# Performance work log

Hardware: AMD Instinct MI355X
Metric: run time of the kernel (lower is better)

## Reference

```python
import jax, jax.numpy as jnp
import numpy as np

N, E, F_IN, DIM, G = 50000, 800000, 128, 128, 512
NUM_GC_LAYERS = 3
S2S_STEPS = 3


def setup_inputs() -> dict:
    key = jax.random.key(0)
    ks = jax.random.split(key, 17)
    s = 0.05
    rn = lambda k, shape: jax.random.normal(k, shape, jnp.float32) * s
    x = jax.random.normal(ks[0], (N, F_IN), jnp.float32)
    edge_index = jax.random.randint(ks[1], (2, E), 0, N)
    batch = jnp.sort(jax.random.randint(ks[2], (N,), 0, G))
    return dict(
        x=x, edge_index=edge_index, batch=batch,
        lin0_W=rn(ks[3], (DIM, F_IN)), lin0_b=rn(ks[4], (DIM,)),
        gin_W1=rn(ks[5], (DIM, DIM)), gin_b1=rn(ks[6], (DIM,)),
        gin_W2=rn(ks[7], (DIM, DIM)), gin_b2=rn(ks[8], (DIM,)),
        gru_Wih=rn(ks[9], (3 * DIM, DIM)), gru_Whh=rn(ks[10], (3 * DIM, DIM)),
        gru_bih=rn(ks[11], (3 * DIM,)), gru_bhh=rn(ks[12], (3 * DIM,)),
        lstm_Wih=rn(ks[13], (4 * DIM, 2 * DIM)), lstm_Whh=rn(ks[14], (4 * DIM, DIM)),
        lstm_bih=rn(ks[15], (4 * DIM,)), lstm_bhh=rn(ks[16], (4 * DIM,)),
    )


def reference(x, edge_index, batch, lin0_W, lin0_b, gin_W1, gin_b1, gin_W2, gin_b2,
              gru_Wih, gru_Whh, gru_bih, gru_bhh,
              lstm_Wih, lstm_Whh, lstm_bih, lstm_bhh):
    src, dst = edge_index[0], edge_index[1]
    out = jax.nn.relu(x @ lin0_W.T + lin0_b)          # [N, DIM]
    h = out                                            # GRU hidden (seq_len=1, 1 layer)
    for _ in range(NUM_GC_LAYERS):
        # GINConv, eps=0: nn(x + sum_{j in N(i)} x_j); scatter-add over edge list
        aggr = jax.ops.segment_sum(out[src], dst, num_segments=N)
        z = out + aggr
        m = jax.nn.relu(jax.nn.relu(z @ gin_W1.T + gin_b1) @ gin_W2.T + gin_b2)
        # single GRU step (PyTorch gate order: r, z, n)
        gx = m @ gru_Wih.T + gru_bih
        gh = h @ gru_Whh.T + gru_bhh
        gxr, gxz, gxn = jnp.split(gx, 3, axis=-1)
        ghr, ghz, ghn = jnp.split(gh, 3, axis=-1)
        r = jax.nn.sigmoid(gxr + ghr)
        zt = jax.nn.sigmoid(gxz + ghz)
        n = jnp.tanh(gxn + r * ghn)
        h = (1.0 - zt) * n + zt * h
        out = h
    # Set2Set pooling (processing_steps=3), LSTM(2*DIM -> DIM), gate order i,f,g,o
    q_star = jnp.zeros((G, 2 * DIM), x.dtype)
    hl = jnp.zeros((G, DIM), x.dtype)
    cl = jnp.zeros((G, DIM), x.dtype)
    for _ in range(S2S_STEPS):
        gates = q_star @ lstm_Wih.T + lstm_bih + hl @ lstm_Whh.T + lstm_bhh
        i, f, g, o = jnp.split(gates, 4, axis=-1)
        cl = jax.nn.sigmoid(f) * cl + jax.nn.sigmoid(i) * jnp.tanh(g)
        hl = jax.nn.sigmoid(o) * jnp.tanh(cl)
        q = hl                                          # [G, DIM]
        e = jnp.sum(out * q[batch], axis=-1)            # [N] attention logits
        emax = jax.lax.stop_gradient(jax.ops.segment_max(e, batch, num_segments=G))
        emax = jnp.where(jnp.isfinite(emax), emax, 0.0)
        a_num = jnp.exp(e - emax[batch])
        denom = jax.ops.segment_sum(a_num, batch, num_segments=G)
        a = a_num / (denom[batch] + 1e-16)              # per-graph softmax
        rvec = jax.ops.segment_sum(a[:, None] * out, batch, num_segments=G)
        q_star = jnp.concatenate([q, rvec], axis=-1)    # [G, 2*DIM]
    return (q_star, out)
```

## Files before the change

kernel.cpp:

```cpp
#include <hip/hip_runtime.h>
#include <hip/hip_bf16.h>
#include <math.h>

static constexpr int NN  = 50000;
static constexpr int NE  = 800000;
static constexpr int DIM = 128;
static constexpr int NG  = 512;
static constexpr int NBLK = (NN + 255) / 256;

typedef __attribute__((ext_vector_type(8))) short bf16x8;
typedef __attribute__((ext_vector_type(4))) float f32x4;
typedef __attribute__((ext_vector_type(8))) float f32x8;

__device__ __forceinline__ float sigm(float x) {
    return __builtin_amdgcn_rcpf(1.0f + __expf(-x));
}
__device__ __forceinline__ float ftanh(float x) {
    x = fminf(fmaxf(x, -15.f), 15.f);
    float t = __expf(2.f * x);
    return (t - 1.f) * __builtin_amdgcn_rcpf(t + 1.f);
}
__device__ __forceinline__ float b2f(ushort u) { return __uint_as_float(((unsigned)u) << 16); }
__device__ __forceinline__ ushort f2b(float f) {
    __hip_bfloat16 h = __float2bfloat16(f);
    return *reinterpret_cast<ushort*>(&h);
}
__device__ __forceinline__ bf16x8 ldb8(const ushort* p) {
    return *reinterpret_cast<const bf16x8*>(p);
}
__device__ __forceinline__ f32x8 acc8(f32x8 a, uint4 v) {
    a[0] += b2f(v.x & 0xffff); a[1] += b2f(v.x >> 16);
    a[2] += b2f(v.y & 0xffff); a[3] += b2f(v.y >> 16);
    a[4] += b2f(v.z & 0xffff); a[5] += b2f(v.z >> 16);
    a[6] += b2f(v.w & 0xffff); a[7] += b2f(v.w >> 16);
    return a;
}

__global__ __launch_bounds__(256) void k_prep(const float* __restrict__ lin0_W,
                                              const float* __restrict__ gin_W1,
                                              const float* __restrict__ gin_W2,
                                              const float* __restrict__ gru_Wih,
                                              const float* __restrict__ gru_Whh,
                                              const float* __restrict__ gru_bih,
                                              const float* __restrict__ gru_bhh,
                                              const float* __restrict__ lstm_Wih,
                                              const float* __restrict__ lstm_Whh,
                                              const float* __restrict__ lstm_bih,
                                              const float* __restrict__ lstm_bhh,
                                              const int* __restrict__ batch,
                                              ushort* __restrict__ wlin0,
                                              ushort* __restrict__ wg1,
                                              ushort* __restrict__ wg2,
                                              ushort* __restrict__ wihb,
                                              ushort* __restrict__ whhb,
                                              ushort* __restrict__ wrz,
                                              float* __restrict__ brz,
                                              float* __restrict__ wltr,
                                              float* __restrict__ bl,
                                              int* __restrict__ deg,
                                              int* __restrict__ gstart,
                                              float* __restrict__ zf) {
    const int S0 = 16384, S1 = S0 + 16384, S2 = S1 + 16384;
    const int S3 = S2 + 49152, S4 = S3 + 49152, S5 = S4 + 65536;
    const int S6 = S5 + 256, S7 = S6 + 196608, S8 = S7 + 512;
    const int S9 = S8 + (NN + 1), S10 = S9 + (NG + 1), S11 = S10 + 262144;
    int i = blockIdx.x * 256 + threadIdx.x;
    if (i < S0) { wlin0[i] = f2b(lin0_W[i]); }
    else if (i < S1) { int j = i - S0; wg1[j] = f2b(gin_W1[j]); }
    else if (i < S2) { int j = i - S1; wg2[j] = f2b(gin_W2[j]); }
    else if (i < S3) { int j = i - S2; wihb[j] = f2b(gru_Wih[j]); }
    else if (i < S4) { int j = i - S3; whhb[j] = f2b(gru_Whh[j]); }
    else if (i < S5) {
        int j = i - S4; int col = j >> 8, k = j & 255;
        int row = (col >> 7) * 128 + (col & 127);
        wrz[j] = f2b((k < 128) ? gru_Whh[row * 128 + k] : gru_Wih[row * 128 + (k - 128)]);
    }
    else if (i < S6) { int j = i - S5; brz[j] = gru_bih[j] + gru_bhh[j]; }
    else if (i < S7) {
        int j = i - S6; int k = j / 512, col = j % 512;
        wltr[j] = (k < 256) ? lstm_Wih[(size_t)col * 256 + k]
                            : lstm_Whh[(size_t)col * 128 + (k - 256)];
    }
    else if (i < S8) { int j = i - S7; bl[j] = lstm_bih[j] + lstm_bhh[j]; }
    else if (i < S9) { deg[i - S8] = 0; }
    else if (i < S10) {
        int g = i - S9;
        int lo = 0, hi = NN;
        while (lo < hi) { int mid = (lo + hi) >> 1; if (batch[mid] < g) lo = mid + 1; else hi = mid; }
        gstart[g] = lo;
    }
    else if (i < S11) { zf[i - S10] = 0.f; }
}
static constexpr int PREP_TOTAL = 16384 * 3 + 49152 * 2 + 65536 + 256 + 196608 + 512 + (NN + 1) + (NG + 1) + 262144;

__global__ void k_count(const int* __restrict__ dst, int* __restrict__ deg, int e) {
    int i = blockIdx.x * blockDim.x + threadIdx.x;
    if (i < e) atomicAdd(&deg[dst[i]], 1);
}

__global__ __launch_bounds__(256) void k_scan_blk(const int* __restrict__ deg,
                                                  int* __restrict__ part,
                                                  int* __restrict__ blksum) {
    __shared__ int s[256];
    int b = blockIdx.x, t = threadIdx.x;
    int i = b * 256 + t;
    int v = (i < NN) ? deg[i] : 0;
    s[t] = v;
    __syncthreads();
    #pragma unroll
    for (int off = 1; off < 256; off <<= 1) {
        int x = (t >= off) ? s[t - off] : 0;
        __syncthreads();
        s[t] += x;
        __syncthreads();
    }
    if (i < NN) part[i] = s[t] - v;
    if (t == 255) blksum[b] = s[255];
}
__global__ __launch_bounds__(256) void k_scan_top(const int* __restrict__ blksum,
                                                  int* __restrict__ blkoff) {
    __shared__ int s[256];
    int t = threadIdx.x;
    int v = (t < NBLK) ? blksum[t] : 0;
    s[t] = v;
    __syncthreads();
    #pragma unroll
    for (int off = 1; off < 256; off <<= 1) {
        int x = (t >= off) ? s[t - off] : 0;
        __syncthreads();
        s[t] += x;
        __syncthreads();
    }
    if (t < NBLK) blkoff[t] = s[t] - v;
    if (t == NBLK - 1) blkoff[NBLK] = s[t];
}
__global__ __launch_bounds__(256) void k_scan_add(const int* __restrict__ part,
                                                  const int* __restrict__ blkoff,
                                                  int* __restrict__ rowptr,
                                                  int* __restrict__ bcur) {
    int b = blockIdx.x, t = threadIdx.x;
    int i = b * 256 + t;
    if (i < NN) {
        int r = part[i] + blkoff[b];
        rowptr[i] = r;
        if ((i & 255) == 0) bcur[i >> 8] = r;
    }
    if (b == 0 && t == 0) rowptr[NN] = blkoff[NBLK];
}

__global__ __launch_bounds__(256) void k_bucket(const int* __restrict__ src,
                                                const int* __restrict__ dst,
                                                int* __restrict__ bcur,
                                                int2* __restrict__ pairs, int e) {
    __shared__ int lcnt[256];
    __shared__ int lbase[256];
    int tid = threadIdx.x;
    lcnt[tid] = 0;
    __syncthreads();
    int base = blockIdx.x * 4096;
    #pragma unroll
    for (int k = 0; k < 16; ++k) {
        int e0 = base + k * 256 + tid;
        if (e0 < e) atomicAdd(&lcnt[dst[e0] >> 8], 1);
    }
    __syncthreads();
    int cnt = lcnt[tid];
    if (cnt > 0) lbase[tid] = atomicAdd(&bcur[tid], cnt);
    __syncthreads();
    lcnt[tid] = 0;
    __syncthreads();
    #pragma unroll
    for (int k = 0; k < 16; ++k) {
        int e0 = base + k * 256 + tid;
        if (e0 < e) {
            int d = dst[e0];
            int b = d >> 8;
            int off = atomicAdd(&lcnt[b], 1);
            pairs[lbase[b] + off] = make_int2(src[e0], d);
        }
    }
}
__global__ __launch_bounds__(256) void k_fillbkt(const int2* __restrict__ pairs,
                                                 const int* __restrict__ rowptr,
                                                 int* __restrict__ csr) {
    __shared__ int lcur[256];
    int b = blockIdx.x, tid = threadIdx.x;
    int w0 = b << 8;
    int w1 = min(w0 + 256, NN);
    if (w0 + tid < w1) lcur[tid] = rowptr[w0 + tid];
    __syncthreads();
    int r0 = rowptr[w0], r1 = rowptr[w1];
    for (int i = r0 + tid; i < r1; i += 256) {
        int2 p = pairs[i];
        int pos = atomicAdd(&lcur[p.y - w0], 1);
        csr[pos] = p.x;
    }
}

__global__ __launch_bounds__(256) void k_lin0(const float* __restrict__ X,
                                              const ushort* __restrict__ W,
                                              const float* __restrict__ bias,
                                              ushort* __restrict__ AB, int n) {
    int lane = threadIdx.x & 63, wave = threadIdx.x >> 6;
    int c0 = lane & 15, kg = (lane >> 4) * 8;
    int tb0 = wave * 32;
    bf16x8 B[2][4];
    #pragma unroll
    for (int t = 0; t < 2; ++t)
        #pragma unroll
        for (int kk = 0; kk < 4; ++kk)
            B[t][kk] = ldb8(W + (size_t)(tb0 + t * 16 + c0) * 128 + kk * 32 + kg);

    for (int m0 = blockIdx.x * 64; m0 < n; m0 += gridDim.x * 64) {
        f32x4 acc[4][2];
        #pragma unroll
        for (int m = 0; m < 4; ++m) { acc[m][0] = {0,0,0,0}; acc[m][1] = {0,0,0,0}; }
        #pragma unroll
        for (int kk = 0; kk < 4; ++kk) {
            #pragma unroll
            for (int m = 0; m < 4; ++m) {
                int ar = min(m0 + m * 16 + c0, n - 1);
                const float* a = X + (size_t)ar * 128 + kk * 32 + kg;
                float4 x0 = *reinterpret_cast<const float4*>(a);
                float4 x1 = *reinterpret_cast<const float4*>(a + 4);
                bf16x8 af;
                af[0] = (short)f2b(x0.x); af[1] = (short)f2b(x0.y);
                af[2] = (short)f2b(x0.z); af[3] = (short)f2b(x0.w);
                af[4] = (short)f2b(x1.x); af[5] = (short)f2b(x1.y);
                af[6] = (short)f2b(x1.z); af[7] = (short)f2b(x1.w);
                acc[m][0] = __builtin_amdgcn_mfma_f32_16x16x32_bf16(af, B[0][kk], acc[m][0], 0, 0, 0);
                acc[m][1] = __builtin_amdgcn_mfma_f32_16x16x32_bf16(af, B[1][kk], acc[m][1], 0, 0, 0);
            }
        }
        #pragma unroll
        for (int m = 0; m < 4; ++m) {
            int rbase = m0 + m * 16 + ((lane >> 4) << 2);
            #pragma unroll
            for (int t = 0; t < 2; ++t) {
                int col = tb0 + t * 16 + c0;
                float bv = bias[col];
                #pragma unroll
                for (int j = 0; j < 4; ++j) {
                    int row = rbase + j;
                    if (row < n) {
                        float v = fmaxf(acc[m][t][j] + bv, 0.f);
                        AB[(size_t)row * 128 + col] = f2b(v);
                    }
                }
            }
        }
    }
}

__global__ __launch_bounds__(512) void k_aggmlp(const ushort* __restrict__ AB,
                                                const int* __restrict__ rowptr,
                                                const int* __restrict__ csr,
                                                const ushort* __restrict__ W1,
                                                const float* __restrict__ b1,
                                                const ushort* __restrict__ W2,
                                                const float* __restrict__ b2,
                                                ushort* __restrict__ mt, int n) {
    __shared__ ushort Z_lds[32 * 136];
    __shared__ ushort M_lds[32 * 136];
    int tid = threadIdx.x;
    int lane = tid & 63, wave = tid >> 6;
    int c0 = lane & 15, kg = (lane >> 4) * 8;
    int colw = wave * 16 + c0;
    int rj = (lane >> 4) << 2;
    int grow_r = tid >> 4;
    int segi = tid & 15;
    const int stride = gridDim.x * 32;

    bf16x8 B1[4], B2[4];
    #pragma unroll
    for (int kk = 0; kk < 4; ++kk) {
        B1[kk] = ldb8(W1 + (size_t)colw * 128 + kk * 32 + kg);
        B2[kk] = ldb8(W2 + (size_t)colw * 128 + kk * 32 + kg);
    }
    float bv1 = b1[colw], bv2 = b2[colw];
    const uint4* bp = (const uint4*)AB;

    for (int m0 = blockIdx.x * 32; m0 < n; m0 += stride) {
        f32x8 A0 = {0,0,0,0,0,0,0,0};
        int grow = m0 + grow_r;
        if (grow < n) {
            f32x8 A1 = {0,0,0,0,0,0,0,0}, A2 = {0,0,0,0,0,0,0,0}, A3 = {0,0,0,0,0,0,0,0};
            A0 = acc8(A0, bp[(size_t)grow * 16 + segi]);
            int p = rowptr[grow], p1 = rowptr[grow + 1];
            for (; p + 4 <= p1; p += 4) {
                uint4 v0 = bp[(size_t)csr[p + 0] * 16 + segi];
                uint4 v1 = bp[(size_t)csr[p + 1] * 16 + segi];
                uint4 v2 = bp[(size_t)csr[p + 2] * 16 + segi];
                uint4 v3 = bp[(size_t)csr[p + 3] * 16 + segi];
                A0 = acc8(A0, v0); A1 = acc8(A1, v1);
                A2 = acc8(A2, v2); A3 = acc8(A3, v3);
            }
            for (; p < p1; ++p) A0 = acc8(A0, bp[(size_t)csr[p] * 16 + segi]);
            #pragma unroll
            for (int i = 0; i < 8; ++i) A0[i] += A1[i] + A2[i] + A3[i];
        }
        bf16x8 zz;
        #pragma unroll
        for (int i = 0; i < 8; ++i) zz[i] = (short)f2b(A0[i]);
        *reinterpret_cast<bf16x8*>(&Z_lds[grow_r * 136 + segi * 8]) = zz;
        __syncthreads();
        {
            f32x4 a[2] = {{0,0,0,0},{0,0,0,0}};
            #pragma unroll
            for (int kk = 0; kk < 4; ++kk) {
                bf16x8 f0 = *reinterpret_cast<const bf16x8*>(&Z_lds[c0 * 136 + kk * 32 + kg]);
                bf16x8 f1 = *reinterpret_cast<const bf16x8*>(&Z_lds[(16 + c0) * 136 + kk * 32 + kg]);
                a[0] = __builtin_amdgcn_mfma_f32_16x16x32_bf16(f0, B1[kk], a[0], 0, 0, 0);
                a[1] = __builtin_amdgcn_mfma_f32_16x16x32_bf16(f1, B1[kk], a[1], 0, 0, 0);
            }
            #pragma unroll
            for (int m = 0; m < 2; ++m)
                #pragma unroll
                for (int j = 0; j < 4; ++j)
                    M_lds[(m * 16 + rj + j) * 136 + colw] = f2b(fmaxf(a[m][j] + bv1, 0.f));
        }
        __syncthreads();
        {
            f32x4 a[2] = {{0,0,0,0},{0,0,0,0}};
            #pragma unroll
            for (int kk = 0; kk < 4; ++kk) {
                bf16x8 f0 = *reinterpret_cast<const bf16x8*>(&M_lds[c0 * 136 + kk * 32 + kg]);
                bf16x8 f1 = *reinterpret_cast<const bf16x8*>(&M_lds[(16 + c0) * 136 + kk * 32 + kg]);
                a[0] = __builtin_amdgcn_mfma_f32_16x16x32_bf16(f0, B2[kk], a[0], 0, 0, 0);
                a[1] = __builtin_amdgcn_mfma_f32_16x16x32_bf16(f1, B2[kk], a[1], 0, 0, 0);
            }
            #pragma unroll
            for (int m = 0; m < 2; ++m)
                #pragma unroll
                for (int j = 0; j < 4; ++j) {
                    int gr2 = m0 + m * 16 + rj + j;
                    if (gr2 < n)
                        mt[(size_t)gr2 * 128 + colw] = f2b(fmaxf(a[m][j] + bv2, 0.f));
                }
        }
        __syncthreads();
    }
}

template<bool WRITEH>
__global__ __launch_bounds__(512) void k_gru3b(const ushort* __restrict__ ABin,
                                               const ushort* __restrict__ mt,
                                               const ushort* __restrict__ wrz,
                                               const float* __restrict__ brz,
                                               const ushort* __restrict__ Wn,
                                               const ushort* __restrict__ Un,
                                               const float* __restrict__ bin,
                                               const float* __restrict__ bhn,
                                               float* __restrict__ Hf,
                                               ushort* __restrict__ ABout, int n) {
    __shared__ ushort A_lds[32 * 264];
    int tid = threadIdx.x;
    int lane = tid & 63, wave = tid >> 6;
    int c0 = lane & 15, kg = (lane >> 4) * 8;
    int colw = wave * 16 + c0;
    int rj = (lane >> 4) << 2;
    int srow = tid >> 4, scol = (tid & 15) * 8;
    const int stride = gridDim.x * 32;

    bf16x8 Brz[2][8];
    #pragma unroll
    for (int kk = 0; kk < 8; ++kk) {
        Brz[0][kk] = ldb8(wrz + (size_t)(colw) * 256 + kk * 32 + kg);
        Brz[1][kk] = ldb8(wrz + (size_t)(128 + colw) * 256 + kk * 32 + kg);
    }
    bf16x8 Bn[4], Bu[4];
    #pragma unroll
    for (int kk = 0; kk < 4; ++kk) {
        Bn[kk] = ldb8(Wn + (size_t)colw * 128 + kk * 32 + kg);
        Bu[kk] = ldb8(Un + (size_t)colw * 128 + kk * 32 + kg);
    }
    float biN = bin[colw], bhN = bhn[colw];
    float brzR = brz[colw], brzZ = brz[128 + colw];

    int m0 = blockIdx.x * 32;
    bf16x8 ph, pm;
    if (m0 < n) {
        int gr = min(m0 + srow, n - 1);
        ph = ldb8(ABin + (size_t)gr * 128 + scol);
        pm = ldb8(mt + (size_t)gr * 128 + scol);
    }
    for (; m0 < n; m0 += stride) {
        *reinterpret_cast<bf16x8*>(&A_lds[srow * 264 + scol]) = ph;
        *reinterpret_cast<bf16x8*>(&A_lds[srow * 264 + 128 + scol]) = pm;
        __syncthreads();
        int mn = m0 + stride;
        if (mn < n) {
            int gr = min(mn + srow, n - 1);
            ph = ldb8(ABin + (size_t)gr * 128 + scol);
            pm = ldb8(mt + (size_t)gr * 128 + scol);
        }
        f32x4 aR[2] = {{0,0,0,0},{0,0,0,0}};
        f32x4 aZ[2] = {{0,0,0,0},{0,0,0,0}};
        #pragma unroll
        for (int kk = 0; kk < 8; ++kk) {
            bf16x8 f0 = *reinterpret_cast<const bf16x8*>(&A_lds[c0 * 264 + kk * 32 + kg]);
            bf16x8 f1 = *reinterpret_cast<const bf16x8*>(&A_lds[(16 + c0) * 264 + kk * 32 + kg]);
            aR[0] = __builtin_amdgcn_mfma_f32_16x16x32_bf16(f0, Brz[0][kk], aR[0], 0, 0, 0);
            aZ[0] = __builtin_amdgcn_mfma_f32_16x16x32_bf16(f0, Brz[1][kk], aZ[0], 0, 0, 0);
            aR[1] = __builtin_amdgcn_mfma_f32_16x16x32_bf16(f1, Brz[0][kk], aR[1], 0, 0, 0);
            aZ[1] = __builtin_amdgcn_mfma_f32_16x16x32_bf16(f1, Brz[1][kk], aZ[1], 0, 0, 0);
        }
        f32x4 an[2] = {{0,0,0,0},{0,0,0,0}};
        f32x4 au[2] = {{0,0,0,0},{0,0,0,0}};
        #pragma unroll
        for (int kk = 0; kk < 4; ++kk) {
            bf16x8 am0 = *reinterpret_cast<const bf16x8*>(&A_lds[c0 * 264 + 128 + kk * 32 + kg]);
            bf16x8 ah0 = *reinterpret_cast<const bf16x8*>(&A_lds[c0 * 264 + kk * 32 + kg]);
            bf16x8 am1 = *reinterpret_cast<const bf16x8*>(&A_lds[(16 + c0) * 264 + 128 + kk * 32 + kg]);
            bf16x8 ah1 = *reinterpret_cast<const bf16x8*>(&A_lds[(16 + c0) * 264 + kk * 32 + kg]);
            an[0] = __builtin_amdgcn_mfma_f32_16x16x32_bf16(am0, Bn[kk], an[0], 0, 0, 0);
            au[0] = __builtin_amdgcn_mfma_f32_16x16x32_bf16(ah0, Bu[kk], au[0], 0, 0, 0);
            an[1] = __builtin_amdgcn_mfma_f32_16x16x32_bf16(am1, Bn[kk], an[1], 0, 0, 0);
            au[1] = __builtin_amdgcn_mfma_f32_16x16x32_bf16(ah1, Bu[kk], au[1], 0, 0, 0);
        }
        #pragma unroll
        for (int m = 0; m < 2; ++m)
            #pragma unroll
            for (int j = 0; j < 4; ++j) {
                int row = m * 16 + rj + j;
                int grow = m0 + row;
                if (grow < n) {
                    float r  = sigm(aR[m][j] + brzR);
                    float zt = sigm(aZ[m][j] + brzZ);
                    float hold = b2f(A_lds[row * 264 + colw]);
                    float nn = ftanh(an[m][j] + biN + r * (au[m][j] + bhN));
                    float hn = (1.f - zt) * nn + zt * hold;
                    ABout[(size_t)grow * 128 + colw] = f2b(hn);
                    if (WRITEH) Hf[(size_t)grow * 128 + colw] = hn;
                }
            }
        __syncthreads();
    }
}

__global__ __launch_bounds__(512) void k_s2s(const ushort* __restrict__ AB,
                                             const float* __restrict__ Wt,
                                             const float* __restrict__ bl,
                                             const int* __restrict__ gstart,
                                             const float* __restrict__ qstar,
                                             float* __restrict__ hl,
                                             float* __restrict__ cl,
                                             float* __restrict__ qout) {
    int g = blockIdx.x, tid = threadIdx.x, lane = tid & 63, wave = tid >> 6;
    __shared__ float qh[384];
    __shared__ float gbuf[512];
    __shared__ float q[128];
    __shared__ float wm[8];
    __shared__ float sw[8];
    __shared__ float rv[8][128];
    if (tid < 256) qh[tid] = qstar[(size_t)g * 256 + tid];
    else if (tid < 384) qh[tid] = hl[(size_t)g * 128 + (tid - 256)];
    __syncthreads();
    float acc = bl[tid];
    #pragma unroll 8
    for (int k = 0; k < 384; ++k)
        acc += Wt[(size_t)k * 512 + tid] * qh[k];
    gbuf[tid] = acc;
    __syncthreads();
    if (tid < 128) {
        float iv = sigm(gbuf[tid]);
        float fv = sigm(gbuf[128 + tid]);
        float gv = ftanh(gbuf[256 + tid]);
        float ov = sigm(gbuf[384 + tid]);
        float cn = fv * cl[(size_t)g * 128 + tid] + iv * gv;
        cl[(size_t)g * 128 + tid] = cn;
        float hn = ov * ftanh(cn);
        hl[(size_t)g * 128 + tid] = hn;
        q[tid] = hn;
    }
    __syncthreads();
    int s = gstart[g], e = gstart[g + 1];
    float q0 = q[2 * lane], q1 = q[2 * lane + 1];
    float mx = -1e30f, sumw = 0.f, a0 = 0.f, a1 = 0.f;
    for (int node = s + wave; node < e; node += 8) {
        unsigned u = ((const unsigned*)AB)[(size_t)node * 64 + lane];
        float v0 = b2f(u & 0xffff), v1 = b2f(u >> 16);
        float p = v0 * q0 + v1 * q1;
        #pragma unroll
        for (int off = 1; off < 64; off <<= 1) p += __shfl_xor(p, off);
        float nm = fmaxf(mx, p);
        float corr = __expf(mx - nm);
        float wgt = __expf(p - nm);
        sumw = sumw * corr + wgt;
        a0 = a0 * corr + wgt * v0;
        a1 = a1 * corr + wgt * v1;
        mx = nm;
    }
    if (lane == 0) wm[wave] = mx;
    __syncthreads();
    float gm = fmaxf(fmaxf(fmaxf(wm[0], wm[1]), fmaxf(wm[2], wm[3])),
                     fmaxf(fmaxf(wm[4], wm[5]), fmaxf(wm[6], wm[7])));
    float cw = __expf(mx - gm);
    rv[wave][2 * lane] = a0 * cw;
    rv[wave][2 * lane + 1] = a1 * cw;
    if (lane == 0) sw[wave] = sumw * cw;
    __syncthreads();
    if (tid < 128) {
        float r = 0.f, d = 1e-16f;
        #pragma unroll
        for (int wv = 0; wv < 8; ++wv) r += rv[wv][tid];
        #pragma unroll
        for (int wv = 0; wv < 8; ++wv) d += sw[wv];
        qout[(size_t)g * 256 + tid] = q[tid];
        qout[(size_t)g * 256 + 128 + tid] = r / d;
    }
}

extern "C" void kernel_launch(void* const* d_in, const int* in_sizes, int n_in,
                              void* d_out, int out_size, void* d_ws, size_t ws_size,
                              hipStream_t stream) {
    const float* x        = (const float*)d_in[0];
    const int*   ei       = (const int*)d_in[1];
    const int*   batch    = (const int*)d_in[2];
    const float* lin0_W   = (const float*)d_in[3];
    const float* lin0_b   = (const float*)d_in[4];
    const float* gin_W1   = (const float*)d_in[5];
    const float* gin_b1   = (const float*)d_in[6];
    const float* gin_W2   = (const float*)d_in[7];
    const float* gin_b2   = (const float*)d_in[8];
    const float* gru_Wih  = (const float*)d_in[9];
    const float* gru_Whh  = (const float*)d_in[10];
    const float* gru_bih  = (const float*)d_in[11];
    const float* gru_bhh  = (const float*)d_in[12];
    const float* lstm_Wih = (const float*)d_in[13];
    const float* lstm_Whh = (const float*)d_in[14];
    const float* lstm_bih = (const float*)d_in[15];
    const float* lstm_bhh = (const float*)d_in[16];

    float* qstar_out = (float*)d_out;
    float* h         = (float*)d_out + (size_t)NG * 2 * DIM;

    char* w = (char*)d_ws;
    ushort* AB0   = (ushort*)w; w += (size_t)NN * 128 * 2;
    ushort* AB1   = (ushort*)w; w += (size_t)NN * 128 * 2;
    ushort* mt    = (ushort*)w; w += (size_t)NN * 128 * 2;
    ushort* wlin0 = (ushort*)w; w += 16384 * 2;
    ushort* wg1   = (ushort*)w; w += 16384 * 2;
    ushort* wg2   = (ushort*)w; w += 16384 * 2;
    ushort* wihb  = (ushort*)w; w += 49152 * 2;
    ushort* whhb  = (ushort*)w; w += 49152 * 2;
    ushort* wrz   = (ushort*)w; w += 65536 * 2;
    float* brz    = (float*)w;  w += 256 * 4;
    float* wltr   = (float*)w;  w += (size_t)512 * 384 * 4;
    float* bl     = (float*)w;  w += 512 * 4;
    float* qstar  = (float*)w;  w += (size_t)NG * 2 * DIM * 4;
    float* hl     = (float*)w;  w += (size_t)NG * DIM * 4;
    float* cl     = (float*)w;  w += (size_t)NG * DIM * 4;
    int* deg      = (int*)w;    w += (size_t)(NN + 1) * 4;
    int* rowptr   = (int*)w;    w += (size_t)(NN + 1) * 4;
    int* bcur     = (int*)w;    w += 256 * 4;
    int* csr_src  = (int*)w;    w += (size_t)NE * 4;
    int2* pairs   = (int2*)w;   w += (size_t)NE * 8;
    int* gstart   = (int*)w;    w += (size_t)(NG + 1) * 4;
    int* part     = (int*)w;    w += (size_t)NN * 4;
    int* blksum   = (int*)w;    w += (size_t)(NBLK + 1) * 4;
    int* blkoff   = (int*)w;    w += (size_t)(NBLK + 1) * 4;

    const int* src = ei;
    const int* dst = ei + NE;

    k_prep<<<(PREP_TOTAL + 255) / 256, 256, 0, stream>>>(
        lin0_W, gin_W1, gin_W2, gru_Wih, gru_Whh, gru_bih, gru_bhh,
        lstm_Wih, lstm_Whh, lstm_bih, lstm_bhh, batch,
        wlin0, wg1, wg2, wihb, whhb, wrz, brz, wltr, bl, deg, gstart, qstar);

    k_count<<<(NE + 255) / 256, 256, 0, stream>>>(dst, deg, NE);
    k_scan_blk<<<NBLK, 256, 0, stream>>>(deg, part, blksum);
    k_scan_top<<<1, 256, 0, stream>>>(blksum, blkoff);
    k_scan_add<<<NBLK, 256, 0, stream>>>(part, blkoff, rowptr, bcur);
    k_bucket<<<(NE + 4095) / 4096, 256, 0, stream>>>(src, dst, bcur, pairs, NE);
    k_fillbkt<<<NBLK, 256, 0, stream>>>(pairs, rowptr, csr_src);

    k_lin0<<<782, 256, 0, stream>>>(x, wlin0, lin0_b, AB0, NN);

    for (int t = 0; t < 3; ++t) {
        ushort* ABc = (t & 1) ? AB1 : AB0;
        ushort* ABn = (t & 1) ? AB0 : AB1;
        k_aggmlp<<<1024, 512, 0, stream>>>(ABc, rowptr, csr_src,
                                           wg1, gin_b1, wg2, gin_b2, mt, NN);
        if (t < 2)
            k_gru3b<false><<<512, 512, 0, stream>>>(ABc, mt, wrz, brz,
                                                    wihb + 256 * 128, whhb + 256 * 128,
                                                    gru_bih + 256, gru_bhh + 256, h, ABn, NN);
        else
            k_gru3b<true><<<512, 512, 0, stream>>>(ABc, mt, wrz, brz,
                                                   wihb + 256 * 128, whhb + 256 * 128,
                                                   gru_bih + 256, gru_bhh + 256, h, ABn, NN);
    }
    const ushort* ABfin = AB1;

    for (int st = 0; st < 3; ++st)
        k_s2s<<<NG, 512, 0, stream>>>(ABfin, wltr, bl, gstart, qstar, hl, cl,
                                      (st == 2) ? qstar_out : qstar);
}
```

Measured before the change: 398.7 us.

## Build CSR via bucket-level counts and fuse lin0 with bucketing

Replaces per-node degree counting and the three-kernel global scan with per-bucket counts, a single-block scan, and a local degree scan inside the fill kernel that writes rowptr. The bucketing pass and the lin0 GEMM now share one launch using disjoint block ranges. This removes several kernel launches and the global atomics on per-node degrees. The cost is that the fill kernel reads the pairs array twice, and lin0 blocks share the grid with bucketing blocks.

```diff
diff --git a/kernel.cpp b/kernel.cpp
--- a/kernel.cpp
+++ b/kernel.cpp
@@ -57,13 +57,13 @@
                                               float* __restrict__ brz,
                                               float* __restrict__ wltr,
                                               float* __restrict__ bl,
-                                              int* __restrict__ deg,
                                               int* __restrict__ gstart,
-                                              float* __restrict__ zf) {
+                                              float* __restrict__ zf,
+                                              int* __restrict__ bcnt) {
     const int S0 = 16384, S1 = S0 + 16384, S2 = S1 + 16384;
     const int S3 = S2 + 49152, S4 = S3 + 49152, S5 = S4 + 65536;
     const int S6 = S5 + 256, S7 = S6 + 196608, S8 = S7 + 512;
-    const int S9 = S8 + (NN + 1), S10 = S9 + (NG + 1), S11 = S10 + 262144;
+    const int S9 = S8 + (NG + 1), S10 = S9 + 262144, S11 = S10 + 256;
     int i = blockIdx.x * 256 + threadIdx.x;
     if (i < S0) { wlin0[i] = f2b(lin0_W[i]); }
     else if (i < S1) { int j = i - S0; wg1[j] = f2b(gin_W1[j]); }
@@ -82,125 +82,94 @@
                             : lstm_Whh[(size_t)col * 128 + (k - 256)];
     }
     else if (i < S8) { int j = i - S7; bl[j] = lstm_bih[j] + lstm_bhh[j]; }
-    else if (i < S9) { deg[i - S8] = 0; }
-    else if (i < S10) {
-        int g = i - S9;
+    else if (i < S9) {
+        int g = i - S8;
         int lo = 0, hi = NN;
         while (lo < hi) { int mid = (lo + hi) >> 1; if (batch[mid] < g) lo = mid + 1; else hi = mid; }
         gstart[g] = lo;
     }
-    else if (i < S11) { zf[i - S10] = 0.f; }
-}
-static constexpr int PREP_TOTAL = 16384 * 3 + 49152 * 2 + 65536 + 256 + 196608 + 512 + (NN + 1) + (NG + 1) + 262144;
-
-__global__ void k_count(const int* __restrict__ dst, int* __restrict__ deg, int e) {
-    int i = blockIdx.x * blockDim.x + threadIdx.x;
-    if (i < e) atomicAdd(&deg[dst[i]], 1);
-}
-
-__global__ __launch_bounds__(256) void k_scan_blk(const int* __restrict__ deg,
-                                                  int* __restrict__ part,
-                                                  int* __restrict__ blksum) {
-    __shared__ int s[256];
-    int b = blockIdx.x, t = threadIdx.x;
-    int i = b * 256 + t;
-    int v = (i < NN) ? deg[i] : 0;
-    s[t] = v;
-    __syncthreads();
-    #pragma unroll
-    for (int off = 1; off < 256; off <<= 1) {
-        int x = (t >= off) ? s[t - off] : 0;
-        __syncthreads();
-        s[t] += x;
-        __syncthreads();
-    }
-    if (i < NN) part[i] = s[t] - v;
-    if (t == 255) blksum[b] = s[255];
-}
-__global__ __launch_bounds__(256) void k_scan_top(const int* __restrict__ blksum,
-                                                  int* __restrict__ blkoff) {
-    __shared__ int s[256];
-    int t = threadIdx.x;
-    int v = (t < NBLK) ? blksum[t] : 0;
-    s[t] = v;
-    __syncthreads();
-    #pragma unroll
-    for (int off = 1; off < 256; off <<= 1) {
-        int x = (t >= off) ? s[t - off] : 0;
-        __syncthreads();
-        s[t] += x;
-        __syncthreads();
-    }
-    if (t < NBLK) blkoff[t] = s[t] - v;
-    if (t == NBLK - 1) blkoff[NBLK] = s[t];
-}
-__global__ __launch_bounds__(256) void k_scan_add(const int* __restrict__ part,
-                                                  const int* __restrict__ blkoff,
-                                                  int* __restrict__ rowptr,
-                                                  int* __restrict__ bcur) {
-    int b = blockIdx.x, t = threadIdx.x;
-    int i = b * 256 + t;
-    if (i < NN) {
-        int r = part[i] + blkoff[b];
-        rowptr[i] = r;
-        if ((i & 255) == 0) bcur[i >> 8] = r;
-    }
-    if (b == 0 && t == 0) rowptr[NN] = blkoff[NBLK];
-}
-
-__global__ __launch_bounds__(256) void k_bucket(const int* __restrict__ src,
-                                                const int* __restrict__ dst,
-                                                int* __restrict__ bcur,
-                                                int2* __restrict__ pairs, int e) {
-    __shared__ int lcnt[256];
-    __shared__ int lbase[256];
+    else if (i < S10) { zf[i - S9] = 0.f; }
+    else if (i < S11) { bcnt[i - S10] = 0; }
+}
+static constexpr int PREP_TOTAL = 16384 * 3 + 49152 * 2 + 65536 + 256 + 196608 + 512 + (NG + 1) + 262144 + 256;
+
+__global__ __launch_bounds__(256) void k_bcount(const int* __restrict__ dst,
+                                                int* __restrict__ bcnt, int e) {
+    __shared__ int l[256];
     int tid = threadIdx.x;
-    lcnt[tid] = 0;
+    l[tid] = 0;
     __syncthreads();
     int base = blockIdx.x * 4096;
     #pragma unroll
     for (int k = 0; k < 16; ++k) {
         int e0 = base + k * 256 + tid;
-        if (e0 < e) atomicAdd(&lcnt[dst[e0] >> 8], 1);
-    }
-    __syncthreads();
-    int cnt = lcnt[tid];
-    if (cnt > 0) lbase[tid] = atomicAdd(&bcur[tid], cnt);
-    __syncthreads();
-    lcnt[tid] = 0;
+        if (e0 < e) atomicAdd(&l[dst[e0] >> 8], 1);
+    }
+    __syncthreads();
+    if (l[tid] > 0) atomicAdd(&bcnt[tid], l[tid]);
+}
+
+__global__ __launch_bounds__(256) void k_btop(const int* __restrict__ bcnt,
+                                              int* __restrict__ bbase,
+                                              int* __restrict__ bcur) {
+    __shared__ int s[256];
+    int t = threadIdx.x;
+    int v = bcnt[t];
+    s[t] = v;
     __syncthreads();
     #pragma unroll
-    for (int k = 0; k < 16; ++k) {
-        int e0 = base + k * 256 + tid;
-        if (e0 < e) {
-            int d = dst[e0];
-            int b = d >> 8;
-            int off = atomicAdd(&lcnt[b], 1);
-            pairs[lbase[b] + off] = make_int2(src[e0], d);
-        }
-    }
-}
-__global__ __launch_bounds__(256) void k_fillbkt(const int2* __restrict__ pairs,
-                                                 const int* __restrict__ rowptr,
-                                                 int* __restrict__ csr) {
-    __shared__ int lcur[256];
-    int b = blockIdx.x, tid = threadIdx.x;
-    int w0 = b << 8;
-    int w1 = min(w0 + 256, NN);
-    if (w0 + tid < w1) lcur[tid] = rowptr[w0 + tid];
-    __syncthreads();
-    int r0 = rowptr[w0], r1 = rowptr[w1];
-    for (int i = r0 + tid; i < r1; i += 256) {
-        int2 p = pairs[i];
-        int pos = atomicAdd(&lcur[p.y - w0], 1);
-        csr[pos] = p.x;
-    }
-}
-
-__global__ __launch_bounds__(256) void k_lin0(const float* __restrict__ X,
-                                              const ushort* __restrict__ W,
-                                              const float* __restrict__ bias,
-                                              ushort* __restrict__ AB, int n) {
+    for (int off = 1; off < 256; off <<= 1) {
+        int x = (t >= off) ? s[t - off] : 0;
+        __syncthreads();
+        s[t] += x;
+        __syncthreads();
+    }
+    int ex = s[t] - v;
+    bbase[t] = ex;
+    bcur[t] = ex;
+    if (t == 255) bbase[256] = s[255];
+}
+
+__global__ __launch_bounds__(256) void k_bucket_lin0(const int* __restrict__ src,
+                                                     const int* __restrict__ dst,
+                                                     int* __restrict__ bcur,
+                                                     int2* __restrict__ pairs, int e,
+                                                     const float* __restrict__ X,
+                                                     const ushort* __restrict__ W,
+                                                     const float* __restrict__ bias,
+                                                     ushort* __restrict__ AB, int n) {
+    if (blockIdx.x < (unsigned)NBLK) {
+        __shared__ int lcnt[256];
+        __shared__ int lbase[256];
+        int tid = threadIdx.x;
+        lcnt[tid] = 0;
+        __syncthreads();
+        int base = blockIdx.x * 4096;
+        #pragma unroll
+        for (int k = 0; k < 16; ++k) {
+            int e0 = base + k * 256 + tid;
+            if (e0 < e) atomicAdd(&lcnt[dst[e0] >> 8], 1);
+        }
+        __syncthreads();
+        int cnt = lcnt[tid];
+        if (cnt > 0) lbase[tid] = atomicAdd(&bcur[tid], cnt);
+        __syncthreads();
+        lcnt[tid] = 0;
+        __syncthreads();
+        #pragma unroll
+        for (int k = 0; k < 16; ++k) {
+            int e0 = base + k * 256 + tid;
+            if (e0 < e) {
+                int d = dst[e0];
+                int b = d >> 8;
+                int off = atomicAdd(&lcnt[b], 1);
+                pairs[lbase[b] + off] = make_int2(src[e0], d);
+            }
+        }
+        return;
+    }
+    int bid = blockIdx.x - NBLK;
+    int nlb = gridDim.x - NBLK;
     int lane = threadIdx.x & 63, wave = threadIdx.x >> 6;
     int c0 = lane & 15, kg = (lane >> 4) * 8;
     int tb0 = wave * 32;
@@ -211,7 +180,7 @@
         for (int kk = 0; kk < 4; ++kk)
             B[t][kk] = ldb8(W + (size_t)(tb0 + t * 16 + c0) * 128 + kk * 32 + kg);
 
-    for (int m0 = blockIdx.x * 64; m0 < n; m0 += gridDim.x * 64) {
+    for (int m0 = bid * 64; m0 < n; m0 += nlb * 64) {
         f32x4 acc[4][2];
         #pragma unroll
         for (int m = 0; m < 4; ++m) { acc[m][0] = {0,0,0,0}; acc[m][1] = {0,0,0,0}; }
@@ -249,6 +218,43 @@
                 }
             }
         }
+    }
+}
+
+__global__ __launch_bounds__(256) void k_fillbkt2(const int2* __restrict__ pairs,
+                                                  const int* __restrict__ bbase,
+                                                  int* __restrict__ rowptr,
+                                                  int* __restrict__ csr) {
+    __shared__ int lcnt[256];
+    __shared__ int s[256];
+    __shared__ int lcur[256];
+    int b = blockIdx.x, tid = threadIdx.x;
+    int w0 = b << 8;
+    int r0 = bbase[b], r1 = bbase[b + 1];
+    lcnt[tid] = 0;
+    __syncthreads();
+    for (int i = r0 + tid; i < r1; i += 256)
+        atomicAdd(&lcnt[pairs[i].y - w0], 1);
+    __syncthreads();
+    int v = lcnt[tid];
+    s[tid] = v;
+    __syncthreads();
+    #pragma unroll
+    for (int off = 1; off < 256; off <<= 1) {
+        int x = (tid >= off) ? s[tid - off] : 0;
+        __syncthreads();
+        s[tid] += x;
+        __syncthreads();
+    }
+    int ex = r0 + s[tid] - v;
+    lcur[tid] = ex;
+    if (w0 + tid < NN) rowptr[w0 + tid] = ex;
+    if (b == 0 && tid == 0) rowptr[NN] = NE;
+    __syncthreads();
+    for (int i = r0 + tid; i < r1; i += 256) {
+        int2 p = pairs[i];
+        int pos = atomicAdd(&lcur[p.y - w0], 1);
+        csr[pos] = p.x;
     }
 }
 
@@ -551,15 +557,13 @@
     float* qstar  = (float*)w;  w += (size_t)NG * 2 * DIM * 4;
     float* hl     = (float*)w;  w += (size_t)NG * DIM * 4;
     float* cl     = (float*)w;  w += (size_t)NG * DIM * 4;
-    int* deg      = (int*)w;    w += (size_t)(NN + 1) * 4;
     int* rowptr   = (int*)w;    w += (size_t)(NN + 1) * 4;
+    int* bcnt     = (int*)w;    w += 256 * 4;
+    int* bbase    = (int*)w;    w += 257 * 4;
     int* bcur     = (int*)w;    w += 256 * 4;
     int* csr_src  = (int*)w;    w += (size_t)NE * 4;
     int2* pairs   = (int2*)w;   w += (size_t)NE * 8;
     int* gstart   = (int*)w;    w += (size_t)(NG + 1) * 4;
-    int* part     = (int*)w;    w += (size_t)NN * 4;
-    int* blksum   = (int*)w;    w += (size_t)(NBLK + 1) * 4;
-    int* blkoff   = (int*)w;    w += (size_t)(NBLK + 1) * 4;
 
     const int* src = ei;
     const int* dst = ei + NE;
@@ -567,16 +571,13 @@
     k_prep<<<(PREP_TOTAL + 255) / 256, 256, 0, stream>>>(
         lin0_W, gin_W1, gin_W2, gru_Wih, gru_Whh, gru_bih, gru_bhh,
         lstm_Wih, lstm_Whh, lstm_bih, lstm_bhh, batch,
-        wlin0, wg1, wg2, wihb, whhb, wrz, brz, wltr, bl, deg, gstart, qstar);
-
-    k_count<<<(NE + 255) / 256, 256, 0, stream>>>(dst, deg, NE);
-    k_scan_blk<<<NBLK, 256, 0, stream>>>(deg, part, blksum);
-    k_scan_top<<<1, 256, 0, stream>>>(blksum, blkoff);
-    k_scan_add<<<NBLK, 256, 0, stream>>>(part, blkoff, rowptr, bcur);
-    k_bucket<<<(NE + 4095) / 4096, 256, 0, stream>>>(src, dst, bcur, pairs, NE);
-    k_fillbkt<<<NBLK, 256, 0, stream>>>(pairs, rowptr, csr_src);
-
-    k_lin0<<<782, 256, 0, stream>>>(x, wlin0, lin0_b, AB0, NN);
+        wlin0, wg1, wg2, wihb, whhb, wrz, brz, wltr, bl, gstart, qstar, bcnt);
+
+    k_bcount<<<(NE + 4095) / 4096, 256, 0, stream>>>(dst, bcnt, NE);
+    k_btop<<<1, 256, 0, stream>>>(bcnt, bbase, bcur);
+    k_bucket_lin0<<<NBLK + 782, 256, 0, stream>>>(src, dst, bcur, pairs, NE,
+                                                  x, wlin0, lin0_b, AB0, NN);
+    k_fillbkt2<<<NBLK, 256, 0, stream>>>(pairs, bbase, rowptr, csr_src);
 
     for (int t = 0; t < 3; ++t) {
         ushort* ABc = (t & 1) ? AB1 : AB0;
```

Measured after the change: 361.4 us. 9.3% less time.
